# Performance work log

Hardware: AMD Instinct MI355X
Metric: run time of the kernel (lower is better)

The kernel has to match this reference:

```python
import jax, jax.numpy as jnp
import numpy as np

B, L, D = 2, 2048, 1024
H, E = 16, 64  # n_heads, per-head dim (E_q=E_k=E_v)
EPS = 1e-5


def _layernorm(x):
    # fresh nn.LayerNorm each forward: gamma=1, beta=0, eps=1e-5 (biased var)
    mu = jnp.mean(x, axis=-1, keepdims=True)
    var = jnp.mean(jnp.square(x - mu), axis=-1, keepdims=True)
    return (x - mu) * jax.lax.rsqrt(var + EPS)


def setup_inputs() -> dict:
    key = jax.random.key(0)
    ks = jax.random.split(key, 9)
    s_in = 1.0 / np.sqrt(D)
    s_ctx = 1.0 / np.sqrt(H * E)
    return {
        "query": jax.random.normal(ks[0], (B, L, D), jnp.float32),
        "key": jax.random.normal(ks[1], (B, L, D), jnp.float32),
        "value": jax.random.normal(ks[2], (B, L, D), jnp.float32),
        # torch nn.Linear weights are [out_features, in_features]
        "W_Q": jax.random.uniform(ks[3], (H * E, D), jnp.float32, -s_in, s_in),
        "W_K": jax.random.uniform(ks[4], (H * E, D), jnp.float32, -s_in, s_in),
        "W_V": jax.random.uniform(ks[5], (H * E, D), jnp.float32, -s_in, s_in),
        "W_O": jax.random.uniform(ks[6], (D, H * E), jnp.float32, -s_ctx, s_ctx),
        "fc_w": jax.random.uniform(ks[7], (D, D), jnp.float32, -s_in, s_in),
        "fc_b": jax.random.uniform(ks[8], (D,), jnp.float32, -s_in, s_in),
    }


def reference(query, key, value, W_Q, W_K, W_V, W_O, fc_w, fc_b):
    b = query.shape[0]
    # projections -> [B, H, L, E]
    q = (query @ W_Q.T).reshape(b, -1, H, E).transpose(0, 2, 1, 3)
    k = (key @ W_K.T).reshape(b, -1, H, E).transpose(0, 2, 1, 3)
    v = (value @ W_V.T).reshape(b, -1, H, E).transpose(0, 2, 1, 3)
    scores = jnp.einsum('bhqe,bhke->bhqk', q, k) / np.sqrt(E).astype(np.float32)
    A = jax.nn.softmax(scores, axis=-1)                 # [B,H,Lq,Lk]
    ctx = jnp.einsum('bhqk,bhke->bhqe', A, v)           # [B,H,L,E]
    ctx = ctx.transpose(0, 2, 1, 3).reshape(b, -1, H * E)
    attn_out = ctx @ W_O.T                               # dropout = identity (eval)
    x = _layernorm(attn_out + query)
    out = x @ fc_w.T + fc_b                              # dropout = identity (eval)
    out = _layernorm(x + out)
    return out
```

## Files before the change

kernel.cpp:

```cpp
#include <hip/hip_runtime.h>
#include <stdint.h>

typedef unsigned short u16;
typedef __bf16 bf16x8 __attribute__((ext_vector_type(8)));
typedef __bf16 bf16x4 __attribute__((ext_vector_type(4)));
typedef float f32x4 __attribute__((ext_vector_type(4)));

#define MFMA16(a,b,c) __builtin_amdgcn_mfma_f32_16x16x32_bf16((a),(b),(c),0,0,0)

__device__ __forceinline__ bf16x4 pack4(float a, float b, float c, float d){
  bf16x4 r; r[0]=(__bf16)a; r[1]=(__bf16)b; r[2]=(__bf16)c; r[3]=(__bf16)d; return r;
}

__device__ __forceinline__ void gl2lds16(const void* g, void* l){
  __builtin_amdgcn_global_load_lds(
      (const __attribute__((address_space(1))) unsigned int*)g,
      (__attribute__((address_space(3))) unsigned int*)l, 16, 0, 0);
}

__device__ __forceinline__ bf16x8 ldsfrag(const u16* base, int row, int gr){
  return *(const bf16x8*)(base + row * 64 + ((gr ^ (row & 7)) << 3));
}

template<int NB, int BN>
__device__ __forceinline__ void gemm_core(const u16* __restrict__ A,
                                          const u16* __restrict__ Bt,
                                          int N, int K, int mode,
                                          void* __restrict__ Cout,
                                          const float* __restrict__ bias,
                                          float oscale)
{
  constexpr int NF = BN / 32;
  __shared__ u16 Al[NB][128 * 64];
  __shared__ u16 Bl[NB][BN * 64];
  const int tid  = threadIdx.x;
  const int lane = tid & 63;
  const int w    = tid >> 6;
  const int wr   = w >> 1, wc = w & 1;
  const int l15  = lane & 15, g = lane >> 4;
  const int rowBase = blockIdx.y << 7;
  const int colBase = blockIdx.x * BN;

  const int srow = tid >> 3;
  const int swz  = ((tid & 7) ^ (srow & 7)) << 3;
  const u16* Ag = A  + (size_t)(rowBase + srow) * K + swz;
  const u16* Bg = Bt + (size_t)(colBase + srow) * K + swz;

  f32x4 acc[4][NF];
#pragma unroll
  for (int m = 0; m < 4; ++m)
#pragma unroll
    for (int n = 0; n < NF; ++n) acc[m][n] = f32x4{0.f, 0.f, 0.f, 0.f};

  auto stage = [&](int buf, int k0) {
#pragma unroll
    for (int i = 0; i < 4; ++i)
      gl2lds16(Ag + (size_t)(i * 32) * K + k0, Al[buf] + i * 2048 + w * 512);
#pragma unroll
    for (int i = 0; i < BN / 32; ++i)
      gl2lds16(Bg + (size_t)(i * 32) * K + k0, Bl[buf] + i * 2048 + w * 512);
  };
  auto compute = [&](int buf) {
    __builtin_amdgcn_s_setprio(1);
#pragma unroll
    for (int kk = 0; kk < 2; ++kk) {
      bf16x8 af[4], bfr[NF];
#pragma unroll
      for (int m = 0; m < 4; ++m) af[m]  = ldsfrag(Al[buf], wr * 64 + m * 16 + l15, kk * 4 + g);
#pragma unroll
      for (int n = 0; n < NF; ++n) bfr[n] = ldsfrag(Bl[buf], wc * (BN/2) + n * 16 + l15, kk * 4 + g);
#pragma unroll
      for (int m = 0; m < 4; ++m)
#pragma unroll
        for (int n = 0; n < NF; ++n)
          acc[m][n] = MFMA16(af[m], bfr[n], acc[m][n]);
    }
    __builtin_amdgcn_s_setprio(0);
  };

  if (NB == 2) {
    stage(0, 0);
    __syncthreads();
    int cur = 0;
    for (int k0 = 0; k0 < K; k0 += 64) {
      if (k0 + 64 < K) stage(cur ^ 1, k0 + 64);
      compute(cur);
      __syncthreads();
      cur ^= 1;
    }
  } else {
    for (int k0 = 0; k0 < K; k0 += 64) {
      stage(0, k0);
      __syncthreads();
      compute(0);
      __syncthreads();
    }
  }

#pragma unroll
  for (int m = 0; m < 4; ++m) {
#pragma unroll
    for (int n = 0; n < NF; ++n) {
      const int row0 = rowBase + wr * 64 + m * 16 + g * 4;
      const int col  = colBase + wc * (BN/2) + n * 16 + l15;
      if (mode == 1) {
        const int b = row0 >> 11, l = row0 & 2047;
        const int h = col >> 6,  e = col & 63;
        *(bf16x4*)((u16*)Cout + ((size_t)((((b << 4) + h) << 6) | e) << 11) + l) =
            pack4(acc[m][n][0], acc[m][n][1], acc[m][n][2], acc[m][n][3]);
      } else {
        const float bb = (mode == 4) ? bias[col] : 0.f;
#pragma unroll
        for (int r = 0; r < 4; ++r) {
          const int row = row0 + r;
          const float v = acc[m][n][r];
          if (mode == 0) {
            *(__bf16*)((u16*)Cout + (size_t)row * N + col) = (__bf16)(v * oscale);
          } else {
            *(__bf16*)((u16*)Cout + (size_t)row * N + col) = (__bf16)(v + bb);
          }
        }
      }
    }
  }
}

#define QSCALE 0.18033688011112042f

__global__ __launch_bounds__(256) void k_proj(
    const u16* __restrict__ qb, const u16* __restrict__ kb, const u16* __restrict__ vb,
    const u16* __restrict__ wq, const u16* __restrict__ wk, const u16* __restrict__ wv,
    u16* __restrict__ Qp, u16* __restrict__ Kp, u16* __restrict__ Vt)
{
  const int z = blockIdx.z;
  const u16* A = (z == 0) ? qb : (z == 1) ? kb : vb;
  const u16* B = (z == 0) ? wq : (z == 1) ? wk : wv;
  void* C = (z == 0) ? (void*)Qp : (z == 1) ? (void*)Kp : (void*)Vt;
  gemm_core<1, 128>(A, B, 1024, 1024, (z == 2) ? 1 : 0, C, nullptr, (z == 0) ? QSCALE : 1.0f);
}

__global__ __launch_bounds__(256) void k_gemm_o(const u16* __restrict__ A,
                                                const u16* __restrict__ B,
                                                u16* __restrict__ C)
{ gemm_core<2, 64>(A, B, 1024, 1024, 0, (void*)C, nullptr, 1.0f); }

__global__ __launch_bounds__(256) void k_gemm_fc(const u16* __restrict__ A,
                                                 const u16* __restrict__ B,
                                                 u16* __restrict__ C,
                                                 const float* __restrict__ bias)
{ gemm_core<2, 64>(A, B, 1024, 1024, 4, (void*)C, bias, 1.0f); }

__global__ __launch_bounds__(256, 2) void k_attn(const u16* __restrict__ Qp,
                                                 const u16* __restrict__ Kp,
                                                 const u16* __restrict__ Vt,
                                                 u16* __restrict__ ctx)
{
  __shared__ u16 Klds[2][64 * 64];
  __shared__ u16 Vlds[2][64 * 64];
  __shared__ u16 Plds[4][32 * 72];

  const int tid = threadIdx.x, lane = tid & 63, w = tid >> 6;
  const int l15 = lane & 15, g = lane >> 4;
  const int bh = blockIdx.y, b = bh >> 4, h = bh & 15;
  const int q0 = blockIdx.x << 7;

  bf16x8 bq[2][2];
#pragma unroll
  for (int u = 0; u < 2; ++u) {
    const u16* Qr = Qp + (((size_t)((b << 11) + q0 + (w << 5) + (u << 4) + l15)) << 10)
                  + (h << 6) + (g << 3);
    bq[u][0] = *(const bf16x8*)(Qr);
    bq[u][1] = *(const bf16x8*)(Qr + 32);
  }

  const f32x4 zero4 = {0.f, 0.f, 0.f, 0.f};
  f32x4 o0[4], o1[4];
#pragma unroll
  for (int f = 0; f < 4; ++f) { o0[f] = zero4; o1[f] = zero4; }
  float ds0 = 0.f, ds1 = 0.f;

  const int srow = tid >> 3;
  const int swz  = ((tid & 7) ^ (srow & 7)) << 3;
  const u16* Kg = Kp + (((size_t)((b << 11) + srow)) << 10) + (h << 6) + swz;
  const u16* Vg = Vt + (((size_t)((bh << 6) + srow)) << 11) + swz;
  u16* Pw = Plds[w];

  auto stage = [&](int buf, int j0) {
#pragma unroll
    for (int i = 0; i < 2; ++i) {
      gl2lds16(Kg + ((size_t)(j0 + i * 32) << 10), Klds[buf] + i * 2048 + w * 512);
      gl2lds16(Vg + ((size_t)(i * 32) << 11) + j0, Vlds[buf] + i * 2048 + w * 512);
    }
  };

  stage(0, 0);
  __syncthreads();
  int cur = 0;

  for (int j0 = 0; j0 < 2048; j0 += 64) {
    if (j0 + 64 < 2048) stage(cur ^ 1, j0 + 64);

    bf16x8 kf[4][2];
#pragma unroll
    for (int f = 0; f < 4; ++f) {
      kf[f][0] = ldsfrag(Klds[cur], f * 16 + l15, g);
      kf[f][1] = ldsfrag(Klds[cur], f * 16 + l15, 4 + g);
    }
    f32x4 s0[4], s1[4];
    __builtin_amdgcn_s_setprio(1);
#pragma unroll
    for (int f = 0; f < 4; ++f) {
      s0[f] = MFMA16(kf[f][0], bq[0][0], zero4);
      s0[f] = MFMA16(kf[f][1], bq[0][1], s0[f]);
      s1[f] = MFMA16(kf[f][0], bq[1][0], zero4);
      s1[f] = MFMA16(kf[f][1], bq[1][1], s1[f]);
    }
    __builtin_amdgcn_s_setprio(0);

#pragma unroll
    for (int f = 0; f < 4; ++f) {
      const float a0 = __builtin_amdgcn_exp2f(s0[f][0]);
      const float a1 = __builtin_amdgcn_exp2f(s0[f][1]);
      const float a2 = __builtin_amdgcn_exp2f(s0[f][2]);
      const float a3 = __builtin_amdgcn_exp2f(s0[f][3]);
      ds0 += (a0 + a1) + (a2 + a3);
      *(bf16x4*)(Pw + l15 * 72 + f * 16 + (g << 2)) = pack4(a0, a1, a2, a3);
      const float c0 = __builtin_amdgcn_exp2f(s1[f][0]);
      const float c1 = __builtin_amdgcn_exp2f(s1[f][1]);
      const float c2 = __builtin_amdgcn_exp2f(s1[f][2]);
      const float c3 = __builtin_amdgcn_exp2f(s1[f][3]);
      ds1 += (c0 + c1) + (c2 + c3);
      *(bf16x4*)(Pw + (16 + l15) * 72 + f * 16 + (g << 2)) = pack4(c0, c1, c2, c3);
    }
    asm volatile("s_waitcnt lgkmcnt(0)" ::: "memory");
    __builtin_amdgcn_sched_barrier(0);

    bf16x8 vf[4][2];
#pragma unroll
    for (int f = 0; f < 4; ++f) {
      vf[f][0] = ldsfrag(Vlds[cur], f * 16 + l15, g);
      vf[f][1] = ldsfrag(Vlds[cur], f * 16 + l15, 4 + g);
    }
    __builtin_amdgcn_s_setprio(1);
#pragma unroll
    for (int kk = 0; kk < 2; ++kk) {
      const bf16x8 pb0 = *(const bf16x8*)(Pw + l15 * 72 + kk * 32 + (g << 3));
      const bf16x8 pb1 = *(const bf16x8*)(Pw + (16 + l15) * 72 + kk * 32 + (g << 3));
#pragma unroll
      for (int f = 0; f < 4; ++f) {
        o0[f] = MFMA16(vf[f][kk], pb0, o0[f]);
        o1[f] = MFMA16(vf[f][kk], pb1, o1[f]);
      }
    }
    __builtin_amdgcn_s_setprio(0);
    __syncthreads();
    cur ^= 1;
  }

  ds0 += __shfl_xor(ds0, 16, 64);
  ds0 += __shfl_xor(ds0, 32, 64);
  ds1 += __shfl_xor(ds1, 16, 64);
  ds1 += __shfl_xor(ds1, 32, 64);
  const float i0 = 1.0f / ds0, i1 = 1.0f / ds1;
  const size_t r0 = (((size_t)((b << 11) + q0 + (w << 5) + l15)) << 10) + (h << 6);
  const size_t r1 = r0 + (16 << 10);
#pragma unroll
  for (int f = 0; f < 4; ++f) {
    *(bf16x4*)(ctx + r0 + f * 16 + (g << 2)) =
        pack4(o0[f][0] * i0, o0[f][1] * i0, o0[f][2] * i0, o0[f][3] * i0);
    *(bf16x4*)(ctx + r1 + f * 16 + (g << 2)) =
        pack4(o1[f][0] * i1, o1[f][1] * i1, o1[f][2] * i1, o1[f][3] * i1);
  }
}

__device__ __forceinline__ void ln_stats(float4 t, int tid, float& mean, float& inv){
  float s = t.x + t.y + t.z + t.w;
  float q = t.x * t.x + t.y * t.y + t.z * t.z + t.w * t.w;
#pragma unroll
  for (int d = 1; d < 64; d <<= 1) {
    s += __shfl_xor(s, d, 64);
    q += __shfl_xor(q, d, 64);
  }
  __shared__ float ps[4], pq[4];
  const int w = tid >> 6;
  if ((tid & 63) == 0) { ps[w] = s; pq[w] = q; }
  __syncthreads();
  s = ps[0] + ps[1] + ps[2] + ps[3];
  q = pq[0] + pq[1] + pq[2] + pq[3];
  mean = s * (1.0f / 1024.0f);
  const float var = q * (1.0f / 1024.0f) - mean * mean;
  inv = rsqrtf(var + 1e-5f);
}

__global__ __launch_bounds__(256) void k_ln1(const u16* __restrict__ a,
                                             const float* __restrict__ res,
                                             u16* __restrict__ xb)
{
  const int row = blockIdx.x, tid = threadIdx.x;
  const size_t base = (size_t)row << 10;
  const bf16x4 av = ((const bf16x4*)(a + base))[tid];
  const float4 rr = ((const float4*)(res + base))[tid];
  float4 t;
  t.x = (float)av[0] + rr.x; t.y = (float)av[1] + rr.y;
  t.z = (float)av[2] + rr.z; t.w = (float)av[3] + rr.w;
  float mean, inv;
  ln_stats(t, tid, mean, inv);
  ((bf16x4*)(xb + base))[tid] = pack4((t.x - mean) * inv, (t.y - mean) * inv,
                                      (t.z - mean) * inv, (t.w - mean) * inv);
}

__global__ __launch_bounds__(256) void k_ln2(const u16* __restrict__ a,
                                             const u16* __restrict__ res,
                                             float* __restrict__ out)
{
  const int row = blockIdx.x, tid = threadIdx.x;
  const size_t base = (size_t)row << 10;
  const bf16x4 av = ((const bf16x4*)(a + base))[tid];
  const bf16x4 rv = ((const bf16x4*)(res + base))[tid];
  float4 t;
  t.x = (float)av[0] + (float)rv[0]; t.y = (float)av[1] + (float)rv[1];
  t.z = (float)av[2] + (float)rv[2]; t.w = (float)av[3] + (float)rv[3];
  float mean, inv;
  ln_stats(t, tid, mean, inv);
  float4 o;
  o.x = (t.x - mean) * inv; o.y = (t.y - mean) * inv;
  o.z = (t.z - mean) * inv; o.w = (t.w - mean) * inv;
  ((float4*)(out + base))[tid] = o;
}

__global__ __launch_bounds__(256) void k_cvt3(const float* __restrict__ q,
                                              const float* __restrict__ k,
                                              const float* __restrict__ v,
                                              u16* __restrict__ qo,
                                              u16* __restrict__ ko,
                                              u16* __restrict__ vo)
{
  const int z = blockIdx.y;
  const float* src = (z == 0) ? q : (z == 1) ? k : v;
  u16* dst = (z == 0) ? qo : (z == 1) ? ko : vo;
  const int i = blockIdx.x * 256 + threadIdx.x;
  const float4 t = ((const float4*)src)[i];
  ((bf16x4*)dst)[i] = pack4(t.x, t.y, t.z, t.w);
}

__global__ __launch_bounds__(256) void k_cvt5(const float* __restrict__ a0,
                                              const float* __restrict__ a1,
                                              const float* __restrict__ a2,
                                              const float* __restrict__ a3,
                                              const float* __restrict__ a4,
                                              u16* __restrict__ o0, u16* __restrict__ o1,
                                              u16* __restrict__ o2, u16* __restrict__ o3,
                                              u16* __restrict__ o4)
{
  const int z = blockIdx.y;
  const float* src = (z == 0) ? a0 : (z == 1) ? a1 : (z == 2) ? a2 : (z == 3) ? a3 : a4;
  u16* dst = (z == 0) ? o0 : (z == 1) ? o1 : (z == 2) ? o2 : (z == 3) ? o3 : o4;
  const int i = blockIdx.x * 256 + threadIdx.x;
  const float4 t = ((const float4*)src)[i];
  ((bf16x4*)dst)[i] = pack4(t.x, t.y, t.z, t.w);
}

extern "C" void kernel_launch(void* const* d_in, const int* in_sizes, int n_in,
                              void* d_out, int out_size, void* d_ws, size_t ws_size,
                              hipStream_t stream)
{
  (void)in_sizes; (void)n_in; (void)out_size; (void)ws_size;
  const float* query = (const float*)d_in[0];
  const float* key   = (const float*)d_in[1];
  const float* value = (const float*)d_in[2];
  const float* W_Q   = (const float*)d_in[3];
  const float* W_K   = (const float*)d_in[4];
  const float* W_V   = (const float*)d_in[5];
  const float* W_O   = (const float*)d_in[6];
  const float* fc_w  = (const float*)d_in[7];
  const float* fc_b  = (const float*)d_in[8];
  float* out = (float*)d_out;
  char* ws = (char*)d_ws;

  u16*   qb    = (u16*)(ws + 0);
  u16*   kb    = (u16*)(ws + 8388608);
  u16*   vb    = (u16*)(ws + 16777216);
  u16*   wq    = (u16*)(ws + 25165824);
  u16*   wk    = (u16*)(ws + 27262976);
  u16*   wv    = (u16*)(ws + 29360128);
  u16*   wo    = (u16*)(ws + 31457280);
  u16*   fw    = (u16*)(ws + 33554432);
  u16*   Qp    = (u16*)(ws + 35651584);
  u16*   Kp    = (u16*)(ws + 44040192);
  u16*   Vt    = (u16*)(ws + 52428800);
  u16*   ctx   = (u16*)(ws + 60817408);
  u16*   attnb = (u16*)(ws + 69206016);
  u16*   xb    = vb;
  u16*   yb    = qb;

  k_cvt3<<<dim3(4096, 3), 256, 0, stream>>>(query, key, value, qb, kb, vb);
  k_cvt5<<<dim3(1024, 5), 256, 0, stream>>>(W_Q, W_K, W_V, W_O, fc_w, wq, wk, wv, wo, fw);
  k_proj<<<dim3(8, 32, 3), 256, 0, stream>>>(qb, kb, vb, wq, wk, wv, Qp, Kp, Vt);
  k_attn<<<dim3(16, 32), 256, 0, stream>>>(Qp, Kp, Vt, ctx);
  k_gemm_o<<<dim3(16, 32), 256, 0, stream>>>(ctx, wo, attnb);
  k_ln1<<<dim3(4096), 256, 0, stream>>>(attnb, query, xb);
  k_gemm_fc<<<dim3(16, 32), 256, 0, stream>>>(xb, fw, yb, fc_b);
  k_ln2<<<dim3(4096), 256, 0, stream>>>(yb, xb, out);
}
```

Baseline: 155.3 us.

## Triple-buffer attention K/V loads, swizzle P tile, retile QKV projection

The attention kernel moves from double to triple buffering of K/V tiles, with a prefetch distance of two. It replaces the full __syncthreads with a partial vmcnt wait plus a raw barrier, so global loads stay in flight across iterations. The P scratch tile drops its padded 72-element stride for a 64-element stride with XOR swizzling, which saves LDS and aims to avoid bank conflicts. The QKV projection switches to the 2x64 GEMM tiling with twice as many blocks. The extra LDS buffer may lower occupancy, and the hand-counted vmcnt values must match the exact number of outstanding loads.

```diff
diff --git a/kernel.cpp b/kernel.cpp
--- a/kernel.cpp
+++ b/kernel.cpp
@@ -136,7 +136,7 @@
   const u16* A = (z == 0) ? qb : (z == 1) ? kb : vb;
   const u16* B = (z == 0) ? wq : (z == 1) ? wk : wv;
   void* C = (z == 0) ? (void*)Qp : (z == 1) ? (void*)Kp : (void*)Vt;
-  gemm_core<1, 128>(A, B, 1024, 1024, (z == 2) ? 1 : 0, C, nullptr, (z == 0) ? QSCALE : 1.0f);
+  gemm_core<2, 64>(A, B, 1024, 1024, (z == 2) ? 1 : 0, C, nullptr, (z == 0) ? QSCALE : 1.0f);
 }
 
 __global__ __launch_bounds__(256) void k_gemm_o(const u16* __restrict__ A,
@@ -155,12 +155,12 @@
                                                  const u16* __restrict__ Vt,
                                                  u16* __restrict__ ctx)
 {
-  __shared__ u16 Klds[2][64 * 64];
-  __shared__ u16 Vlds[2][64 * 64];
-  __shared__ u16 Plds[4][32 * 72];
+  __shared__ u16 Klds[3][64 * 64];
+  __shared__ u16 Vlds[3][64 * 64];
+  __shared__ u16 Plds[4][32 * 64];
 
   const int tid = threadIdx.x, lane = tid & 63, w = tid >> 6;
-  const int l15 = lane & 15, g = lane >> 4;
+  const int l15 = lane & 15, g = lane >> 4, l7 = l15 & 7;
   const int bh = blockIdx.y, b = bh >> 4, h = bh & 15;
   const int q0 = blockIdx.x << 7;
 
@@ -194,11 +194,16 @@
   };
 
   stage(0, 0);
-  __syncthreads();
+  stage(1, 64);
+  asm volatile("s_waitcnt vmcnt(4)" ::: "memory");
+  __builtin_amdgcn_s_barrier();
+
   int cur = 0;
-
-  for (int j0 = 0; j0 < 2048; j0 += 64) {
-    if (j0 + 64 < 2048) stage(cur ^ 1, j0 + 64);
+  for (int t = 0; t < 32; ++t) {
+    if (t + 2 < 32) {
+      int nb = cur + 2; if (nb >= 3) nb -= 3;
+      stage(nb, (t + 2) << 6);
+    }
 
     bf16x8 kf[4][2];
 #pragma unroll
@@ -224,13 +229,15 @@
       const float a2 = __builtin_amdgcn_exp2f(s0[f][2]);
       const float a3 = __builtin_amdgcn_exp2f(s0[f][3]);
       ds0 += (a0 + a1) + (a2 + a3);
-      *(bf16x4*)(Pw + l15 * 72 + f * 16 + (g << 2)) = pack4(a0, a1, a2, a3);
+      *(bf16x4*)(Pw + l15 * 64 + ((((2 * f) + (g >> 1)) ^ l7) << 3) + ((g & 1) << 2)) =
+          pack4(a0, a1, a2, a3);
       const float c0 = __builtin_amdgcn_exp2f(s1[f][0]);
       const float c1 = __builtin_amdgcn_exp2f(s1[f][1]);
       const float c2 = __builtin_amdgcn_exp2f(s1[f][2]);
       const float c3 = __builtin_amdgcn_exp2f(s1[f][3]);
       ds1 += (c0 + c1) + (c2 + c3);
-      *(bf16x4*)(Pw + (16 + l15) * 72 + f * 16 + (g << 2)) = pack4(c0, c1, c2, c3);
+      *(bf16x4*)(Pw + (16 + l15) * 64 + ((((2 * f) + (g >> 1)) ^ l7) << 3) + ((g & 1) << 2)) =
+          pack4(c0, c1, c2, c3);
     }
     asm volatile("s_waitcnt lgkmcnt(0)" ::: "memory");
     __builtin_amdgcn_sched_barrier(0);
@@ -244,8 +251,8 @@
     __builtin_amdgcn_s_setprio(1);
 #pragma unroll
     for (int kk = 0; kk < 2; ++kk) {
-      const bf16x8 pb0 = *(const bf16x8*)(Pw + l15 * 72 + kk * 32 + (g << 3));
-      const bf16x8 pb1 = *(const bf16x8*)(Pw + (16 + l15) * 72 + kk * 32 + (g << 3));
+      const bf16x8 pb0 = *(const bf16x8*)(Pw + l15 * 64 + (((kk * 4 + g) ^ l7) << 3));
+      const bf16x8 pb1 = *(const bf16x8*)(Pw + (16 + l15) * 64 + (((kk * 4 + g) ^ l7) << 3));
 #pragma unroll
       for (int f = 0; f < 4; ++f) {
         o0[f] = MFMA16(vf[f][kk], pb0, o0[f]);
@@ -253,8 +260,15 @@
       }
     }
     __builtin_amdgcn_s_setprio(0);
-    __syncthreads();
-    cur ^= 1;
+
+    if (t + 2 < 32) {
+      asm volatile("s_waitcnt vmcnt(4)" ::: "memory");
+      __builtin_amdgcn_s_barrier();
+    } else if (t + 1 < 32) {
+      asm volatile("s_waitcnt vmcnt(0)" ::: "memory");
+      __builtin_amdgcn_s_barrier();
+    }
+    ++cur; if (cur >= 3) cur -= 3;
   }
 
   ds0 += __shfl_xor(ds0, 16, 64);
@@ -395,7 +409,7 @@
 
   k_cvt3<<<dim3(4096, 3), 256, 0, stream>>>(query, key, value, qb, kb, vb);
   k_cvt5<<<dim3(1024, 5), 256, 0, stream>>>(W_Q, W_K, W_V, W_O, fc_w, wq, wk, wv, wo, fw);
-  k_proj<<<dim3(8, 32, 3), 256, 0, stream>>>(qb, kb, vb, wq, wk, wv, Qp, Kp, Vt);
+  k_proj<<<dim3(16, 32, 3), 256, 0, stream>>>(qb, kb, vb, wq, wk, wv, Qp, Kp, Vt);
   k_attn<<<dim3(16, 32), 256, 0, stream>>>(Qp, Kp, Vt, ctx);
   k_gemm_o<<<dim3(16, 32), 256, 0, stream>>>(ctx, wo, attnb);
   k_ln1<<<dim3(4096), 256, 0, stream>>>(attnb, query, xb);
```

Result: no change. 156.3 us (+0.6%).
